# Optimization experiments

Hardware: AMD Instinct MI355X
Metric: run time of the kernel (lower is better)

## Reference

```python
import jax, jax.numpy as jnp
import numpy as np

C = 64          # channel multiplicity of node irreps (64x0e + 64x1o)
N = 10000       # nodes
E = 160000      # edges
F_EDGE = 8      # edge radial features (8x0e)
N_ELEM = 10     # one-hot element types (node_attrs, unused by this block)
WNUM = 4 * C    # conv_tp.weight_numel: 4 uvu instructions x 64 channels
SQ3 = float(np.sqrt(3.0))


def split_feats(x):
    # e3nn flat layout: [64 scalars | 64 vectors x 3 (u-major)]
    s = x[:, :C]
    v = x[:, C:].reshape(-1, C, 3)
    return s, v


def o3_linear(s, v, W0, W1):
    # per-irrep channel mixing with 1/sqrt(fan_in) normalization
    inv = 1.0 / float(np.sqrt(C))
    return (s @ W0) * inv, jnp.einsum('ncm,cd->ndm', v, W1) * inv


def fc_net(x, ws):
    # e3nn FullyConnectedNet: silu MLP with 1/sqrt(fan_in) scaling, no act on last
    for w in ws[:-1]:
        x = jax.nn.silu((x @ w) / float(np.sqrt(w.shape[0])))
    w = ws[-1]
    return (x @ w) / float(np.sqrt(w.shape[0]))


def setup_inputs() -> dict:
    key = jax.random.key(0)
    ks = jax.random.split(key, 16)
    inp = {}
    inp['node_attrs'] = jax.random.normal(ks[0], (N, N_ELEM), jnp.float32)
    inp['node_feats'] = jax.random.normal(ks[1], (N, C + 3 * C), jnp.float32)
    inp['edge_attrs'] = jax.random.normal(ks[2], (E, 4), jnp.float32)
    inp['edge_feats'] = jax.random.normal(ks[3], (E, F_EDGE), jnp.float32)
    inp['edge_index'] = jax.random.randint(ks[4], (2, E), 0, N, jnp.int32)
    inp['edge_vectors'] = jax.random.normal(ks[5], (E, 3), jnp.float32)
    inp['batch'] = jax.random.randint(ks[6], (N,), 0, 16, jnp.int32)
    inp['num_graphs'] = 16
    # learned params
    inp['W1_0'] = jax.random.normal(ks[7], (C, C), jnp.float32)
    inp['W1_1'] = jax.random.normal(ks[8], (C, C), jnp.float32)
    inp['W2_0'] = jax.random.normal(ks[9], (C, C), jnp.float32)
    inp['W2_1'] = jax.random.normal(ks[10], (C, C), jnp.float32)
    inp['fc_w0'] = jax.random.normal(ks[11], (F_EDGE, 64), jnp.float32)
    inp['fc_w1'] = jax.random.normal(ks[12], (64, 64), jnp.float32)
    inp['fc_w2'] = jax.random.normal(ks[13], (64, 64), jnp.float32)
    inp['fc_w3'] = jax.random.normal(ks[14], (64, WNUM), jnp.float32)
    k15, k16 = jax.random.split(ks[15])
    inp['Wf'] = jax.random.normal(k15, (2 * C, 1), jnp.float32)   # 128x0e mid -> 1x0e
    inp['Wm1'] = jax.random.normal(k16, (C, 1), jnp.float32)      # 64x1o -> 1x1o multipole
    return inp


def reference(node_attrs, node_feats, edge_attrs, edge_feats, edge_index,
              edge_vectors, batch, num_graphs,
              W1_0, W1_1, W2_0, W2_1, fc_w0, fc_w1, fc_w2, fc_w3, Wf, Wm1):
    sender = edge_index[0]
    receiver = edge_index[1]

    # per-edge tensor-product weights from radial features: [E, 4*C]
    tp_w = fc_net(edge_feats, [fc_w0, fc_w1, fc_w2, fc_w3])
    w0, w1, w2, w3 = (tp_w[:, 0 * C:1 * C], tp_w[:, 1 * C:2 * C],
                      tp_w[:, 2 * C:3 * C], tp_w[:, 3 * C:4 * C])

    s, v = split_feats(node_feats)
    s1, v1 = o3_linear(s, v, W1_0, W1_1)
    s2, v2 = o3_linear(s, v, W2_0, W2_1)

    # gather + symmetric bond features
    bs = s1[sender] + s2[receiver]          # [E, C] scalars
    bv = v1[sender] + v2[receiver]          # [E, C, 3] vectors

    y0 = edge_attrs[:, 0]                   # l=0 edge attr
    y1 = edge_attrs[:, 1:4]                 # l=1 edge attr

    # CG tensor product (uvu, shared_weights=False): only scalar (0e) outputs of
    # irreps_mid reach the final 1x0e o3.Linear, so the 1o paths drop out exactly.
    m0a = w0 * bs * y0[:, None]                                  # 0e x 0e -> 0e
    m0b = w3 * (jnp.einsum('ecm,em->ec', bv, y1) / SQ3)          # 1o x 1o -> 0e

    # final o3.Linear (128x0e -> 1x0e) and /40 scaling
    mid0 = jnp.concatenate([m0a, m0b], axis=-1)                  # [E, 2C]
    p_ji = (mid0 @ Wf)[:, 0] / float(np.sqrt(2 * C)) / 40.0      # [E]

    # double scatter-sum: antisymmetric charge transfer
    charges = (jax.ops.segment_sum(p_ji, receiver, num_segments=N)
               - jax.ops.segment_sum(p_ji, sender, num_segments=N))

    # multipole block: 0e component zeroed then overwritten by charges
    mvec = jnp.einsum('ncm,cd->ndm', v, Wm1)[:, 0, :] / float(np.sqrt(C))  # [N, 3]
    multipoles = jnp.concatenate([charges[:, None], mvec], axis=-1)        # [N, 4]

    return multipoles, p_ji[:, None]
```

## Files before the change

kernel.cpp:

```cpp
#include <hip/hip_runtime.h>
#include <hip/hip_bf16.h>

typedef float v4f __attribute__((ext_vector_type(4)));
typedef float f32x4 __attribute__((ext_vector_type(4)));
typedef unsigned short u16;
typedef unsigned short us4 __attribute__((ext_vector_type(4)));
typedef unsigned short us8 __attribute__((ext_vector_type(8)));
typedef short s16x8 __attribute__((ext_vector_type(8)));

#define N_NODES 10000
#define N_EDGES 160000

#define SWZ(idx, row) ((idx) ^ (((row) & 7) << 3))
#define GIDX(r, o) (((r) << 8) + (((((o) >> 3) ^ ((r) & 7))) << 3) + ((o) & 7))

__device__ __forceinline__ u16 f2b(float x) {
  union { float f; unsigned u; } v; v.f = x;
  unsigned r = v.u + 0x7fffu + ((v.u >> 16) & 1u);
  return (u16)(r >> 16);
}
__device__ __forceinline__ float b2f(u16 u) {
  union { unsigned u; float f; } v; v.u = ((unsigned)u) << 16; return v.f;
}
__device__ __forceinline__ float silu_f(float x) { return x / (1.0f + __expf(-x)); }

__device__ __forceinline__ void bar_lgkm() {
  asm volatile("s_waitcnt lgkmcnt(0)" ::: "memory");
  __builtin_amdgcn_s_barrier();
}

__device__ __forceinline__ void gload_lds16(const u16* g, u16* l) {
  __builtin_amdgcn_global_load_lds(
      (const __attribute__((address_space(1))) unsigned int*)g,
      (__attribute__((address_space(3))) unsigned int*)l, 16, 0, 0);
}

__global__ __launch_bounds__(256) void prep_kernel(
    const float* __restrict__ fcw0,
    const float* __restrict__ fcw1, const float* __restrict__ fcw2,
    const float* __restrict__ fcw3,
    const float* __restrict__ W10, const float* __restrict__ W20,
    const float* __restrict__ W11, const float* __restrict__ W21,
    u16* __restrict__ prep, float* __restrict__ out)
{
  const int fid = blockIdx.x * 256 + threadIdx.x;
  for (int i = fid; i < N_NODES; i += 4352) out[(size_t)i * 4] = 0.f;
  int f, sec;
  if (fid < 512)       { sec = 0; f = fid; }
  else if (fid < 1024) { sec = 1; f = fid - 512; }
  else if (fid < 2048) { sec = 2; f = fid - 1024; }
  else if (fid < 3072) { sec = 3; f = fid - 2048; }
  else if (fid < 4096) { sec = 4; f = fid - 3072; }
  else                 { sec = 5; f = fid - 4096; }
  const int lane = f & 63;
  us8 vals;
  if (sec == 5) {
    const int ut = f >> 6;
    #pragma unroll
    for (int j = 0; j < 8; ++j) {
      const int k = (lane >> 4) * 8 + j;
      vals[j] = (k < 8) ? f2b(fcw0[k * 64 + ut * 16 + (lane & 15)]) : (u16)0;
    }
  } else {
    const int kw = (f >> 6) & 1, ut = f >> 7;
    #pragma unroll
    for (int j = 0; j < 8; ++j) {
      const int k = kw * 32 + (lane >> 4) * 8 + j;
      float v;
      if (sec == 0) v = fcw1[k * 64 + ut * 16 + (lane & 15)];
      else if (sec == 1) v = fcw2[k * 64 + ut * 16 + (lane & 15)];
      else if (sec == 2) {
        const int col = (ut < 4) ? (ut * 16 + (lane & 15)) : (192 + (ut - 4) * 16 + (lane & 15));
        v = fcw3[k * 256 + col];
      } else if (sec == 3) {
        const int u = ut * 16 + (lane & 15);
        v = (u < 64) ? W10[k * 64 + u] : W20[k * 64 + (u - 64)];
      } else {
        const int u = ut * 16 + (lane & 15);
        v = (u < 64) ? W11[k * 64 + u] : W21[k * 64 + (u - 64)];
      }
      vals[j] = f2b(v);
    }
  }
  *(us8*)&prep[(size_t)fid * 8] = vals;
}

__global__ __launch_bounds__(256) void node_kernel(
    const float* __restrict__ nf,
    const u16* __restrict__ prepNS, const u16* __restrict__ prepNV,
    const float* __restrict__ Wm1,
    u16* __restrict__ Atab, u16* __restrict__ Btab, float* __restrict__ out)
{
  __shared__ u16 Ss[1024];
  __shared__ u16 Vs[3][1024];
  __shared__ float wm1s[64];
  const int tid = threadIdx.x, w = tid >> 6, lane = tid & 63;
  const int nb = blockIdx.x;

  if (tid < 64) wm1s[tid] = Wm1[tid];
  #pragma unroll
  for (int it = 0; it < 4; ++it) {
    const int flat = it * 1024 + tid * 4;
    const int nl = flat >> 8;
    const int col = flat & 255;
    const v4f x = *(const v4f*)&nf[((size_t)(nb * 16 + nl)) * 256 + col];
    #pragma unroll
    for (int i = 0; i < 4; ++i) {
      const int c2 = col + i;
      const u16 b = f2b(x[i]);
      if (c2 < 64) Ss[SWZ(nl * 64 + c2, nl)] = b;
      else {
        const int cc = c2 - 64, c = cc / 3, m = cc - c * 3;
        Vs[m][SWZ(nl * 64 + c, nl)] = b;
      }
    }
  }
  __syncthreads();

  const int nr = lane & 15, kg = (lane >> 4) * 8;
  const u16* plane = (w == 0) ? Ss : Vs[w - 1];
  const u16* pw = (w == 0) ? prepNS : prepNV;
  const s16x8 b0 = *(const s16x8*)&plane[SWZ(nr * 64 + kg, nr)];
  const s16x8 b1 = *(const s16x8*)&plane[SWZ(nr * 64 + 32 + kg, nr)];
  const int node = nb * 16 + nr;
  #pragma unroll
  for (int utg = 0; utg < 8; ++utg) {
    const s16x8 a0 = *(const s16x8*)&pw[((utg * 2 + 0) * 64 + lane) * 8];
    const s16x8 a1 = *(const s16x8*)&pw[((utg * 2 + 1) * 64 + lane) * 8];
    f32x4 acc = {0.f, 0.f, 0.f, 0.f};
    acc = __builtin_amdgcn_mfma_f32_16x16x32_bf16(a0, b0, acc, 0, 0, 0);
    acc = __builtin_amdgcn_mfma_f32_16x16x32_bf16(a1, b1, acc, 0, 0, 0);
    us4 st;
    #pragma unroll
    for (int j = 0; j < 4; ++j) st[j] = f2b(acc[j] * 0.125f);
    u16* tab = (utg < 4) ? Atab : Btab;
    const int ch = w * 64 + (utg & 3) * 16 + (lane >> 4) * 4;
    *(us4*)&tab[(size_t)node * 256 + ch] = st;
  }

  if (tid < 192) {
    const int task = tid >> 2, sub = tid & 3;
    const int nl3 = task / 3, m = task - nl3 * 3;
    float acc = 0.f;
    #pragma unroll
    for (int i = 0; i < 16; ++i) {
      const int c = sub * 16 + i;
      acc += b2f(Vs[m][SWZ(nl3 * 64 + c, nl3)]) * wm1s[c];
    }
    acc += __shfl_xor(acc, 1);
    acc += __shfl_xor(acc, 2);
    if (sub == 0) out[(nb * 16 + nl3) * 4 + 1 + m] = acc * 0.125f;
  }
}

__device__ __forceinline__ void mfma_layer32(const u16* Hin, u16* Hout,
                                             s16x8 a0, s16x8 a1, int w, int lane) {
  const int er = lane & 15, kg = (lane >> 4) * 8;
  __builtin_amdgcn_s_setprio(1);
  #pragma unroll
  for (int et = 0; et < 2; ++et) {
    const int e = et * 16 + er;
    const s16x8 b0 = *(const s16x8*)&Hin[SWZ(e * 64 + kg, e)];
    const s16x8 b1 = *(const s16x8*)&Hin[SWZ(e * 64 + 32 + kg, e)];
    f32x4 acc = {0.f, 0.f, 0.f, 0.f};
    acc = __builtin_amdgcn_mfma_f32_16x16x32_bf16(a0, b0, acc, 0, 0, 0);
    acc = __builtin_amdgcn_mfma_f32_16x16x32_bf16(a1, b1, acc, 0, 0, 0);
    us4 st;
    #pragma unroll
    for (int j = 0; j < 4; ++j) st[j] = f2b(silu_f(acc[j] * 0.125f));
    *(us4*)&Hout[SWZ(e * 64 + w * 16 + (lane >> 4) * 4, e)] = st;
  }
  __builtin_amdgcn_s_setprio(0);
}

__global__ __launch_bounds__(256, 2) void edge_kernel(
    const float* __restrict__ edge_attrs,
    const float* __restrict__ edge_feats,
    const int*   __restrict__ edge_index,
    const u16*   __restrict__ prep,
    const float* __restrict__ Wf,
    const u16*   __restrict__ Atab, const u16* __restrict__ Btab,
    float* __restrict__ out, float* __restrict__ p_out)
{
  __shared__ u16 G[2][16384];
  __shared__ u16 HA[2048], HB[2048];
  __shared__ u16 F16[256];
  __shared__ float yL[4][32];
  __shared__ float Psum[128];

  const int tid = threadIdx.x, w = tid >> 6, lane = tid & 63;
  const int half = lane >> 5, l31 = lane & 31;
  const int er = lane & 15, kg = (lane >> 4) * 8;
  const int cb = w * 16 + (lane >> 4) * 4;
  const int eb0 = blockIdx.x * 128;

  const u16* pL2 = prep;
  const u16* pL3 = prep + 512 * 8;
  const u16* pL4 = prep + 1024 * 8;
  const s16x8 a2_0 = *(const s16x8*)&pL2[((w * 2 + 0) * 64 + lane) * 8];
  const s16x8 a2_1 = *(const s16x8*)&pL2[((w * 2 + 1) * 64 + lane) * 8];
  const s16x8 a3_0 = *(const s16x8*)&pL3[((w * 2 + 0) * 64 + lane) * 8];
  const s16x8 a3_1 = *(const s16x8*)&pL3[((w * 2 + 1) * 64 + lane) * 8];
  const s16x8 as0 = *(const s16x8*)&pL4[((w * 2 + 0) * 64 + lane) * 8];
  const s16x8 as1 = *(const s16x8*)&pL4[((w * 2 + 1) * 64 + lane) * 8];
  const s16x8 av0 = *(const s16x8*)&pL4[(((4 + w) * 2 + 0) * 64 + lane) * 8];
  const s16x8 av1 = *(const s16x8*)&pL4[(((4 + w) * 2 + 1) * 64 + lane) * 8];
  const s16x8 a1w = *(const s16x8*)&prep[(size_t)(4096 + w * 64 + lane) * 8];
  const v4f wfA = *(const v4f*)&Wf[cb];
  v4f wfB = *(const v4f*)&Wf[64 + cb];
  #pragma unroll
  for (int j = 0; j < 4; ++j) wfB[j] *= 0.5773502691896258f;

  const u16* tabW = (w < 2) ? Atab : Btab;
  const int  eoff = (w < 2) ? 0 : N_EDGES;

  int nidx[2][8];
  int sndR[2], rcvR[2];
  v4f eaR[2], f0R[2], f1R[2];

  {
    #pragma unroll
    for (int i = 0; i < 8; ++i)
      nidx[0][i] = edge_index[eoff + eb0 + (w & 1) * 16 + 2 * i + half];
    if (tid < 32) {
      sndR[0] = edge_index[eb0 + tid];
      rcvR[0] = edge_index[N_EDGES + eb0 + tid];
      eaR[0] = *(const v4f*)&edge_attrs[(size_t)(eb0 + tid) * 4];
      f0R[0] = *(const v4f*)&edge_feats[(size_t)(eb0 + tid) * 8];
      f1R[0] = *(const v4f*)&edge_feats[(size_t)(eb0 + tid) * 8 + 4];
    }
    asm volatile("s_waitcnt vmcnt(0)" ::: "memory");
    #pragma unroll
    for (int i = 0; i < 8; ++i) {
      const int grow = w * 16 + 2 * i + half;
      const u16* src = tabW + (size_t)nidx[0][i] * 256 + (size_t)((l31 ^ (grow & 7)) << 3);
      gload_lds16(src, &G[0][(w * 16 + 2 * i) * 256]);
    }
    __builtin_amdgcn_sched_barrier(0);
    if (tid < 32) {
      yL[0][tid] = eaR[0][0]; yL[1][tid] = eaR[0][1];
      yL[2][tid] = eaR[0][2]; yL[3][tid] = eaR[0][3];
      us8 o;
      #pragma unroll
      for (int k = 0; k < 4; ++k) { o[k] = f2b(f0R[0][k]); o[4 + k] = f2b(f1R[0][k]); }
      *(us8*)&F16[tid * 8] = o;
    }
    bar_lgkm();
  }

  #pragma unroll
  for (int t = 0; t < 4; ++t) {
    const int cur = t & 1, nxt = cur ^ 1;
    const int eb = eb0 + t * 32;

    if (t < 3) {
      const int ebn = eb + 32;
      #pragma unroll
      for (int i = 0; i < 8; ++i)
        nidx[nxt][i] = edge_index[eoff + ebn + (w & 1) * 16 + 2 * i + half];
      if (tid < 32) {
        sndR[nxt] = edge_index[ebn + tid];
        rcvR[nxt] = edge_index[N_EDGES + ebn + tid];
        eaR[nxt] = *(const v4f*)&edge_attrs[(size_t)(ebn + tid) * 4];
        f0R[nxt] = *(const v4f*)&edge_feats[(size_t)(ebn + tid) * 8];
        f1R[nxt] = *(const v4f*)&edge_feats[(size_t)(ebn + tid) * 8 + 4];
      }
      __builtin_amdgcn_sched_barrier(0);
    }

    {
      __builtin_amdgcn_s_setprio(1);
      #pragma unroll
      for (int et = 0; et < 2; ++et) {
        s16x8 bF = {0, 0, 0, 0, 0, 0, 0, 0};
        if (lane < 16) bF = *(const s16x8*)&F16[(et * 16 + lane) * 8];
        f32x4 acc = {0.f, 0.f, 0.f, 0.f};
        acc = __builtin_amdgcn_mfma_f32_16x16x32_bf16(a1w, bF, acc, 0, 0, 0);
        const int e = et * 16 + er;
        us4 st;
        #pragma unroll
        for (int j = 0; j < 4; ++j)
          st[j] = f2b(silu_f(acc[j] * 0.35355339059327373f));
        *(us4*)&HA[SWZ(e * 64 + w * 16 + (lane >> 4) * 4, e)] = st;
      }
      __builtin_amdgcn_s_setprio(0);
    }
    bar_lgkm();
    mfma_layer32(HA, HB, a2_0, a2_1, w, lane);
    bar_lgkm();
    mfma_layer32(HB, HA, a3_0, a3_1, w, lane);
    bar_lgkm();

    f32x4 accS[2], accV[2];
    __builtin_amdgcn_s_setprio(1);
    #pragma unroll
    for (int et = 0; et < 2; ++et) {
      const int e = et * 16 + er;
      const s16x8 b0 = *(const s16x8*)&HA[SWZ(e * 64 + kg, e)];
      const s16x8 b1 = *(const s16x8*)&HA[SWZ(e * 64 + 32 + kg, e)];
      f32x4 aS = {0.f,0.f,0.f,0.f}, aV = {0.f,0.f,0.f,0.f};
      aS = __builtin_amdgcn_mfma_f32_16x16x32_bf16(as0, b0, aS, 0, 0, 0);
      aS = __builtin_amdgcn_mfma_f32_16x16x32_bf16(as1, b1, aS, 0, 0, 0);
      aV = __builtin_amdgcn_mfma_f32_16x16x32_bf16(av0, b0, aV, 0, 0, 0);
      aV = __builtin_amdgcn_mfma_f32_16x16x32_bf16(av1, b1, aV, 0, 0, 0);
      accS[et] = aS; accV[et] = aV;
    }
    __builtin_amdgcn_s_setprio(0);

    asm volatile("s_waitcnt vmcnt(0)" ::: "memory");
    if (t < 3) {
      #pragma unroll
      for (int i = 0; i < 8; ++i) {
        const int grow = w * 16 + 2 * i + half;
        const u16* src = tabW + (size_t)nidx[nxt][i] * 256 + (size_t)((l31 ^ (grow & 7)) << 3);
        gload_lds16(src, &G[nxt][(w * 16 + 2 * i) * 256]);
      }
      __builtin_amdgcn_sched_barrier(0);
    }
    __builtin_amdgcn_s_barrier();

    #pragma unroll
    for (int et = 0; et < 2; ++et) {
      const int e = et * 16 + er;
      const int rA = e, rB = 32 + e;
      const us4 As = *(const us4*)&G[cur][GIDX(rA, cb)];
      const us4 Ax = *(const us4*)&G[cur][GIDX(rA, 64 + cb)];
      const us4 Ay = *(const us4*)&G[cur][GIDX(rA, 128 + cb)];
      const us4 Az = *(const us4*)&G[cur][GIDX(rA, 192 + cb)];
      const us4 Bs = *(const us4*)&G[cur][GIDX(rB, cb)];
      const us4 Bx = *(const us4*)&G[cur][GIDX(rB, 64 + cb)];
      const us4 By = *(const us4*)&G[cur][GIDX(rB, 128 + cb)];
      const us4 Bz = *(const us4*)&G[cur][GIDX(rB, 192 + cb)];
      const float y0 = yL[0][e], yx = yL[1][e], yy = yL[2][e], yz = yL[3][e];
      float part = 0.f;
      #pragma unroll
      for (int j = 0; j < 4; ++j) {
        const float bs = b2f(As[j]) + b2f(Bs[j]);
        const float bv = (b2f(Ax[j]) + b2f(Bx[j])) * yx +
                         (b2f(Ay[j]) + b2f(By[j])) * yy +
                         (b2f(Az[j]) + b2f(Bz[j])) * yz;
        part += accS[et][j] * bs * y0 * wfA[j] + accV[et][j] * bv * wfB[j];
      }
      part += __shfl_xor(part, 16);
      part += __shfl_xor(part, 32);
      if (lane < 16) Psum[w * 32 + et * 16 + lane] = part;
    }
    bar_lgkm();
    if (tid < 32) {
      const float p = (Psum[tid] + Psum[32 + tid] + Psum[64 + tid] + Psum[96 + tid])
                      * 2.7621358640766505e-4f;
      p_out[eb + tid] = p;
      atomicAdd(&out[(size_t)rcvR[cur] * 4], p);
      atomicAdd(&out[(size_t)sndR[cur] * 4], -p);
      if (t < 3) {
        yL[0][tid] = eaR[nxt][0]; yL[1][tid] = eaR[nxt][1];
        yL[2][tid] = eaR[nxt][2]; yL[3][tid] = eaR[nxt][3];
        us8 o;
        #pragma unroll
        for (int k = 0; k < 4; ++k) { o[k] = f2b(f0R[nxt][k]); o[4 + k] = f2b(f1R[nxt][k]); }
        *(us8*)&F16[tid * 8] = o;
      }
    }
    bar_lgkm();
  }
}

extern "C" void kernel_launch(void* const* d_in, const int* in_sizes, int n_in,
                              void* d_out, int out_size, void* d_ws, size_t ws_size,
                              hipStream_t stream) {
  const float* node_feats = (const float*)d_in[1];
  const float* edge_attrs = (const float*)d_in[2];
  const float* edge_feats = (const float*)d_in[3];
  const int*   edge_index = (const int*)d_in[4];
  const float* W10  = (const float*)d_in[8];
  const float* W11  = (const float*)d_in[9];
  const float* W20  = (const float*)d_in[10];
  const float* W21  = (const float*)d_in[11];
  const float* fcw0 = (const float*)d_in[12];
  const float* fcw1 = (const float*)d_in[13];
  const float* fcw2 = (const float*)d_in[14];
  const float* fcw3 = (const float*)d_in[15];
  const float* Wf   = (const float*)d_in[16];
  const float* Wm1  = (const float*)d_in[17];
  float* out = (float*)d_out;

  char* ws = (char*)d_ws;
  u16* Atab = (u16*)ws;
  u16* Btab = (u16*)(ws + 5120000);
  u16* prep = (u16*)(ws + 10240000);

  prep_kernel<<<17, 256, 0, stream>>>(fcw0, fcw1, fcw2, fcw3, W10, W20, W11, W21,
                                      prep, out);
  node_kernel<<<625, 256, 0, stream>>>(node_feats, prep + 2048 * 8, prep + 3072 * 8,
                                       Wm1, Atab, Btab, out);
  edge_kernel<<<1250, 256, 0, stream>>>(edge_attrs, edge_feats, edge_index,
                                        prep, Wf, Atab, Btab,
                                        out, out + 40000);
}
```

Baseline: 156.3 us.

## Gather node rows directly into registers instead of double-buffered LDS staging

Removes the 64KB double-buffered LDS gather of per-edge sender/receiver table rows, which used global_load_lds. Each lane now loads only the 4-element slices it needs straight into registers at the start of each tile, and these loads overlap with the radial MLP MFMAs. This cuts LDS usage and one barrier per tile, which may allow higher occupancy. In exchange, prefetch is no longer one tile ahead: gather latency is hidden only within the same tile, and the scattered 8-byte loads are less coalesced than before.

```diff
diff --git a/kernel.cpp b/kernel.cpp
--- a/kernel.cpp
+++ b/kernel.cpp
@@ -12,7 +12,6 @@
 #define N_EDGES 160000
 
 #define SWZ(idx, row) ((idx) ^ (((row) & 7) << 3))
-#define GIDX(r, o) (((r) << 8) + (((((o) >> 3) ^ ((r) & 7))) << 3) + ((o) & 7))
 
 __device__ __forceinline__ u16 f2b(float x) {
   union { float f; unsigned u; } v; v.f = x;
@@ -27,12 +26,6 @@
 __device__ __forceinline__ void bar_lgkm() {
   asm volatile("s_waitcnt lgkmcnt(0)" ::: "memory");
   __builtin_amdgcn_s_barrier();
-}
-
-__device__ __forceinline__ void gload_lds16(const u16* g, u16* l) {
-  __builtin_amdgcn_global_load_lds(
-      (const __attribute__((address_space(1))) unsigned int*)g,
-      (__attribute__((address_space(3))) unsigned int*)l, 16, 0, 0);
 }
 
 __global__ __launch_bounds__(256) void prep_kernel(
@@ -182,14 +175,12 @@
     const u16*   __restrict__ Atab, const u16* __restrict__ Btab,
     float* __restrict__ out, float* __restrict__ p_out)
 {
-  __shared__ u16 G[2][16384];
   __shared__ u16 HA[2048], HB[2048];
   __shared__ u16 F16[256];
   __shared__ float yL[4][32];
   __shared__ float Psum[128];
 
   const int tid = threadIdx.x, w = tid >> 6, lane = tid & 63;
-  const int half = lane >> 5, l31 = lane & 31;
   const int er = lane & 15, kg = (lane >> 4) * 8;
   const int cb = w * 16 + (lane >> 4) * 4;
   const int eb0 = blockIdx.x * 128;
@@ -211,38 +202,28 @@
   #pragma unroll
   for (int j = 0; j < 4; ++j) wfB[j] *= 0.5773502691896258f;
 
-  const u16* tabW = (w < 2) ? Atab : Btab;
-  const int  eoff = (w < 2) ? 0 : N_EDGES;
-
-  int nidx[2][8];
+  int sndv[2][2], rcvv[2][2];
   int sndR[2], rcvR[2];
-  v4f eaR[2], f0R[2], f1R[2];
+  v4f eaR, f0R, f1R;
+  us4 gA[2][4], gB[2][4];
 
   {
     #pragma unroll
-    for (int i = 0; i < 8; ++i)
-      nidx[0][i] = edge_index[eoff + eb0 + (w & 1) * 16 + 2 * i + half];
+    for (int et = 0; et < 2; ++et) {
+      sndv[0][et] = edge_index[eb0 + et * 16 + er];
+      rcvv[0][et] = edge_index[N_EDGES + eb0 + et * 16 + er];
+    }
     if (tid < 32) {
       sndR[0] = edge_index[eb0 + tid];
       rcvR[0] = edge_index[N_EDGES + eb0 + tid];
-      eaR[0] = *(const v4f*)&edge_attrs[(size_t)(eb0 + tid) * 4];
-      f0R[0] = *(const v4f*)&edge_feats[(size_t)(eb0 + tid) * 8];
-      f1R[0] = *(const v4f*)&edge_feats[(size_t)(eb0 + tid) * 8 + 4];
-    }
-    asm volatile("s_waitcnt vmcnt(0)" ::: "memory");
-    #pragma unroll
-    for (int i = 0; i < 8; ++i) {
-      const int grow = w * 16 + 2 * i + half;
-      const u16* src = tabW + (size_t)nidx[0][i] * 256 + (size_t)((l31 ^ (grow & 7)) << 3);
-      gload_lds16(src, &G[0][(w * 16 + 2 * i) * 256]);
-    }
-    __builtin_amdgcn_sched_barrier(0);
-    if (tid < 32) {
-      yL[0][tid] = eaR[0][0]; yL[1][tid] = eaR[0][1];
-      yL[2][tid] = eaR[0][2]; yL[3][tid] = eaR[0][3];
+      eaR = *(const v4f*)&edge_attrs[(size_t)(eb0 + tid) * 4];
+      f0R = *(const v4f*)&edge_feats[(size_t)(eb0 + tid) * 8];
+      f1R = *(const v4f*)&edge_feats[(size_t)(eb0 + tid) * 8 + 4];
+      yL[0][tid] = eaR[0]; yL[1][tid] = eaR[1];
+      yL[2][tid] = eaR[2]; yL[3][tid] = eaR[3];
       us8 o;
       #pragma unroll
-      for (int k = 0; k < 4; ++k) { o[k] = f2b(f0R[0][k]); o[4 + k] = f2b(f1R[0][k]); }
+      for (int k = 0; k < 4; ++k) { o[k] = f2b(f0R[k]); o[4 + k] = f2b(f1R[k]); }
       *(us8*)&F16[tid * 8] = o;
     }
     bar_lgkm();
@@ -253,17 +234,31 @@
     const int cur = t & 1, nxt = cur ^ 1;
     const int eb = eb0 + t * 32;
 
+    #pragma unroll
+    for (int et = 0; et < 2; ++et) {
+      const u16* ra = Atab + (size_t)sndv[cur][et] * 256 + cb;
+      const u16* rb = Btab + (size_t)rcvv[cur][et] * 256 + cb;
+      #pragma unroll
+      for (int sec = 0; sec < 4; ++sec) {
+        gA[et][sec] = *(const us4*)&ra[sec * 64];
+        gB[et][sec] = *(const us4*)&rb[sec * 64];
+      }
+    }
+    __builtin_amdgcn_sched_barrier(0);
+
     if (t < 3) {
       const int ebn = eb + 32;
       #pragma unroll
-      for (int i = 0; i < 8; ++i)
-        nidx[nxt][i] = edge_index[eoff + ebn + (w & 1) * 16 + 2 * i + half];
+      for (int et = 0; et < 2; ++et) {
+        sndv[nxt][et] = edge_index[ebn + et * 16 + er];
+        rcvv[nxt][et] = edge_index[N_EDGES + ebn + et * 16 + er];
+      }
       if (tid < 32) {
         sndR[nxt] = edge_index[ebn + tid];
         rcvR[nxt] = edge_index[N_EDGES + ebn + tid];
-        eaR[nxt] = *(const v4f*)&edge_attrs[(size_t)(ebn + tid) * 4];
-        f0R[nxt] = *(const v4f*)&edge_feats[(size_t)(ebn + tid) * 8];
-        f1R[nxt] = *(const v4f*)&edge_feats[(size_t)(ebn + tid) * 8 + 4];
+        eaR = *(const v4f*)&edge_attrs[(size_t)(ebn + tid) * 4];
+        f0R = *(const v4f*)&edge_feats[(size_t)(ebn + tid) * 8];
+        f1R = *(const v4f*)&edge_feats[(size_t)(ebn + tid) * 8 + 4];
       }
       __builtin_amdgcn_sched_barrier(0);
     }
@@ -308,37 +303,18 @@
     __builtin_amdgcn_s_setprio(0);
 
     asm volatile("s_waitcnt vmcnt(0)" ::: "memory");
-    if (t < 3) {
-      #pragma unroll
-      for (int i = 0; i < 8; ++i) {
-        const int grow = w * 16 + 2 * i + half;
-        const u16* src = tabW + (size_t)nidx[nxt][i] * 256 + (size_t)((l31 ^ (grow & 7)) << 3);
-        gload_lds16(src, &G[nxt][(w * 16 + 2 * i) * 256]);
-      }
-      __builtin_amdgcn_sched_barrier(0);
-    }
-    __builtin_amdgcn_s_barrier();
 
     #pragma unroll
     for (int et = 0; et < 2; ++et) {
       const int e = et * 16 + er;
-      const int rA = e, rB = 32 + e;
-      const us4 As = *(const us4*)&G[cur][GIDX(rA, cb)];
-      const us4 Ax = *(const us4*)&G[cur][GIDX(rA, 64 + cb)];
-      const us4 Ay = *(const us4*)&G[cur][GIDX(rA, 128 + cb)];
-      const us4 Az = *(const us4*)&G[cur][GIDX(rA, 192 + cb)];
-      const us4 Bs = *(const us4*)&G[cur][GIDX(rB, cb)];
-      const us4 Bx = *(const us4*)&G[cur][GIDX(rB, 64 + cb)];
-      const us4 By = *(const us4*)&G[cur][GIDX(rB, 128 + cb)];
-      const us4 Bz = *(const us4*)&G[cur][GIDX(rB, 192 + cb)];
       const float y0 = yL[0][e], yx = yL[1][e], yy = yL[2][e], yz = yL[3][e];
       float part = 0.f;
       #pragma unroll
       for (int j = 0; j < 4; ++j) {
-        const float bs = b2f(As[j]) + b2f(Bs[j]);
-        const float bv = (b2f(Ax[j]) + b2f(Bx[j])) * yx +
-                         (b2f(Ay[j]) + b2f(By[j])) * yy +
-                         (b2f(Az[j]) + b2f(Bz[j])) * yz;
+        const float bs = b2f(gA[et][0][j]) + b2f(gB[et][0][j]);
+        const float bv = (b2f(gA[et][1][j]) + b2f(gB[et][1][j])) * yx +
+                         (b2f(gA[et][2][j]) + b2f(gB[et][2][j])) * yy +
+                         (b2f(gA[et][3][j]) + b2f(gB[et][3][j])) * yz;
         part += accS[et][j] * bs * y0 * wfA[j] + accV[et][j] * bv * wfB[j];
       }
       part += __shfl_xor(part, 16);
@@ -346,6 +322,7 @@
       if (lane < 16) Psum[w * 32 + et * 16 + lane] = part;
     }
     bar_lgkm();
+
     if (tid < 32) {
       const float p = (Psum[tid] + Psum[32 + tid] + Psum[64 + tid] + Psum[96 + tid])
                       * 2.7621358640766505e-4f;
@@ -353,11 +330,11 @@
       atomicAdd(&out[(size_t)rcvR[cur] * 4], p);
       atomicAdd(&out[(size_t)sndR[cur] * 4], -p);
       if (t < 3) {
-        yL[0][tid] = eaR[nxt][0]; yL[1][tid] = eaR[nxt][1];
-        yL[2][tid] = eaR[nxt][2]; yL[3][tid] = eaR[nxt][3];
+        yL[0][tid] = eaR[0]; yL[1][tid] = eaR[1];
+        yL[2][tid] = eaR[2]; yL[3][tid] = eaR[3];
         us8 o;
         #pragma unroll
-        for (int k = 0; k < 4; ++k) { o[k] = f2b(f0R[nxt][k]); o[4 + k] = f2b(f1R[nxt][k]); }
+        for (int k = 0; k < 4; ++k) { o[k] = f2b(f0R[k]); o[4 + k] = f2b(f1R[k]); }
         *(us8*)&F16[tid * 8] = o;
       }
     }
```

Result: slower. 166.2 us (+6.3%).

## Single-buffer gathered node tables in edge kernel and double tiles per block

Applied to the files above, without the earlier changes.

The gathered-node LDS buffer goes from two buffers to one, so each block uses about 32 KB less shared memory. The gather for the next tile is now issued only after the current tile's reads have finished. Each block also handles 8 edge tiles instead of 4, halving the grid to 625 blocks. The aim is higher occupancy from the smaller LDS footprint and less per-block setup, at the cost of losing overlap of the gather with the MFMA work inside one block, which now has to come from other resident blocks.

```diff
diff --git a/kernel.cpp b/kernel.cpp
--- a/kernel.cpp
+++ b/kernel.cpp
@@ -10,6 +10,7 @@
 
 #define N_NODES 10000
 #define N_EDGES 160000
+#define NTILE 8
 
 #define SWZ(idx, row) ((idx) ^ (((row) & 7) << 3))
 #define GIDX(r, o) (((r) << 8) + (((((o) >> 3) ^ ((r) & 7))) << 3) + ((o) & 7))
@@ -182,7 +183,7 @@
     const u16*   __restrict__ Atab, const u16* __restrict__ Btab,
     float* __restrict__ out, float* __restrict__ p_out)
 {
-  __shared__ u16 G[2][16384];
+  __shared__ u16 G[16384];
   __shared__ u16 HA[2048], HB[2048];
   __shared__ u16 F16[256];
   __shared__ float yL[4][32];
@@ -192,7 +193,7 @@
   const int half = lane >> 5, l31 = lane & 31;
   const int er = lane & 15, kg = (lane >> 4) * 8;
   const int cb = w * 16 + (lane >> 4) * 4;
-  const int eb0 = blockIdx.x * 128;
+  const int eb0 = blockIdx.x * (NTILE * 32);
 
   const u16* pL2 = prep;
   const u16* pL3 = prep + 512 * 8;
@@ -216,7 +217,7 @@
 
   int nidx[2][8];
   int sndR[2], rcvR[2];
-  v4f eaR[2], f0R[2], f1R[2];
+  v4f eaR, f0R, f1R;
 
   {
     #pragma unroll
@@ -225,35 +226,35 @@
     if (tid < 32) {
       sndR[0] = edge_index[eb0 + tid];
       rcvR[0] = edge_index[N_EDGES + eb0 + tid];
-      eaR[0] = *(const v4f*)&edge_attrs[(size_t)(eb0 + tid) * 4];
-      f0R[0] = *(const v4f*)&edge_feats[(size_t)(eb0 + tid) * 8];
-      f1R[0] = *(const v4f*)&edge_feats[(size_t)(eb0 + tid) * 8 + 4];
+      eaR = *(const v4f*)&edge_attrs[(size_t)(eb0 + tid) * 4];
+      f0R = *(const v4f*)&edge_feats[(size_t)(eb0 + tid) * 8];
+      f1R = *(const v4f*)&edge_feats[(size_t)(eb0 + tid) * 8 + 4];
     }
     asm volatile("s_waitcnt vmcnt(0)" ::: "memory");
     #pragma unroll
     for (int i = 0; i < 8; ++i) {
       const int grow = w * 16 + 2 * i + half;
       const u16* src = tabW + (size_t)nidx[0][i] * 256 + (size_t)((l31 ^ (grow & 7)) << 3);
-      gload_lds16(src, &G[0][(w * 16 + 2 * i) * 256]);
+      gload_lds16(src, &G[(w * 16 + 2 * i) * 256]);
     }
     __builtin_amdgcn_sched_barrier(0);
     if (tid < 32) {
-      yL[0][tid] = eaR[0][0]; yL[1][tid] = eaR[0][1];
-      yL[2][tid] = eaR[0][2]; yL[3][tid] = eaR[0][3];
+      yL[0][tid] = eaR[0]; yL[1][tid] = eaR[1];
+      yL[2][tid] = eaR[2]; yL[3][tid] = eaR[3];
       us8 o;
       #pragma unroll
-      for (int k = 0; k < 4; ++k) { o[k] = f2b(f0R[0][k]); o[4 + k] = f2b(f1R[0][k]); }
+      for (int k = 0; k < 4; ++k) { o[k] = f2b(f0R[k]); o[4 + k] = f2b(f1R[k]); }
       *(us8*)&F16[tid * 8] = o;
     }
     bar_lgkm();
   }
 
   #pragma unroll
-  for (int t = 0; t < 4; ++t) {
+  for (int t = 0; t < NTILE; ++t) {
     const int cur = t & 1, nxt = cur ^ 1;
     const int eb = eb0 + t * 32;
 
-    if (t < 3) {
+    if (t < NTILE - 1) {
       const int ebn = eb + 32;
       #pragma unroll
       for (int i = 0; i < 8; ++i)
@@ -261,9 +262,9 @@
       if (tid < 32) {
         sndR[nxt] = edge_index[ebn + tid];
         rcvR[nxt] = edge_index[N_EDGES + ebn + tid];
-        eaR[nxt] = *(const v4f*)&edge_attrs[(size_t)(ebn + tid) * 4];
-        f0R[nxt] = *(const v4f*)&edge_feats[(size_t)(ebn + tid) * 8];
-        f1R[nxt] = *(const v4f*)&edge_feats[(size_t)(ebn + tid) * 8 + 4];
+        eaR = *(const v4f*)&edge_attrs[(size_t)(ebn + tid) * 4];
+        f0R = *(const v4f*)&edge_feats[(size_t)(ebn + tid) * 8];
+        f1R = *(const v4f*)&edge_feats[(size_t)(ebn + tid) * 8 + 4];
       }
       __builtin_amdgcn_sched_barrier(0);
     }
@@ -308,29 +309,20 @@
     __builtin_amdgcn_s_setprio(0);
 
     asm volatile("s_waitcnt vmcnt(0)" ::: "memory");
-    if (t < 3) {
-      #pragma unroll
-      for (int i = 0; i < 8; ++i) {
-        const int grow = w * 16 + 2 * i + half;
-        const u16* src = tabW + (size_t)nidx[nxt][i] * 256 + (size_t)((l31 ^ (grow & 7)) << 3);
-        gload_lds16(src, &G[nxt][(w * 16 + 2 * i) * 256]);
-      }
-      __builtin_amdgcn_sched_barrier(0);
-    }
     __builtin_amdgcn_s_barrier();
 
     #pragma unroll
     for (int et = 0; et < 2; ++et) {
       const int e = et * 16 + er;
       const int rA = e, rB = 32 + e;
-      const us4 As = *(const us4*)&G[cur][GIDX(rA, cb)];
-      const us4 Ax = *(const us4*)&G[cur][GIDX(rA, 64 + cb)];
-      const us4 Ay = *(const us4*)&G[cur][GIDX(rA, 128 + cb)];
-      const us4 Az = *(const us4*)&G[cur][GIDX(rA, 192 + cb)];
-      const us4 Bs = *(const us4*)&G[cur][GIDX(rB, cb)];
-      const us4 Bx = *(const us4*)&G[cur][GIDX(rB, 64 + cb)];
-      const us4 By = *(const us4*)&G[cur][GIDX(rB, 128 + cb)];
-      const us4 Bz = *(const us4*)&G[cur][GIDX(rB, 192 + cb)];
+      const us4 As = *(const us4*)&G[GIDX(rA, cb)];
+      const us4 Ax = *(const us4*)&G[GIDX(rA, 64 + cb)];
+      const us4 Ay = *(const us4*)&G[GIDX(rA, 128 + cb)];
+      const us4 Az = *(const us4*)&G[GIDX(rA, 192 + cb)];
+      const us4 Bs = *(const us4*)&G[GIDX(rB, cb)];
+      const us4 Bx = *(const us4*)&G[GIDX(rB, 64 + cb)];
+      const us4 By = *(const us4*)&G[GIDX(rB, 128 + cb)];
+      const us4 Bz = *(const us4*)&G[GIDX(rB, 192 + cb)];
       const float y0 = yL[0][e], yx = yL[1][e], yy = yL[2][e], yz = yL[3][e];
       float part = 0.f;
       #pragma unroll
@@ -346,18 +338,29 @@
       if (lane < 16) Psum[w * 32 + et * 16 + lane] = part;
     }
     bar_lgkm();
+
+    if (t < NTILE - 1) {
+      #pragma unroll
+      for (int i = 0; i < 8; ++i) {
+        const int grow = w * 16 + 2 * i + half;
+        const u16* src = tabW + (size_t)nidx[nxt][i] * 256 + (size_t)((l31 ^ (grow & 7)) << 3);
+        gload_lds16(src, &G[(w * 16 + 2 * i) * 256]);
+      }
+      __builtin_amdgcn_sched_barrier(0);
+    }
+
     if (tid < 32) {
       const float p = (Psum[tid] + Psum[32 + tid] + Psum[64 + tid] + Psum[96 + tid])
                       * 2.7621358640766505e-4f;
       p_out[eb + tid] = p;
       atomicAdd(&out[(size_t)rcvR[cur] * 4], p);
       atomicAdd(&out[(size_t)sndR[cur] * 4], -p);
-      if (t < 3) {
-        yL[0][tid] = eaR[nxt][0]; yL[1][tid] = eaR[nxt][1];
-        yL[2][tid] = eaR[nxt][2]; yL[3][tid] = eaR[nxt][3];
+      if (t < NTILE - 1) {
+        yL[0][tid] = eaR[0]; yL[1][tid] = eaR[1];
+        yL[2][tid] = eaR[2]; yL[3][tid] = eaR[3];
         us8 o;
         #pragma unroll
-        for (int k = 0; k < 4; ++k) { o[k] = f2b(f0R[nxt][k]); o[4 + k] = f2b(f1R[nxt][k]); }
+        for (int k = 0; k < 4; ++k) { o[k] = f2b(f0R[k]); o[4 + k] = f2b(f1R[k]); }
         *(us8*)&F16[tid * 8] = o;
       }
     }
@@ -393,7 +396,7 @@
                                       prep, out);
   node_kernel<<<625, 256, 0, stream>>>(node_feats, prep + 2048 * 8, prep + 3072 * 8,
                                        Wm1, Atab, Btab, out);
-  edge_kernel<<<1250, 256, 0, stream>>>(edge_attrs, edge_feats, edge_index,
-                                        prep, Wf, Atab, Btab,
-                                        out, out + 40000);
-}
+  edge_kernel<<<625, 256, 0, stream>>>(edge_attrs, edge_feats, edge_index,
+                                       prep, Wf, Atab, Btab,
+                                       out, out + 40000);
+}
```

Result: faster. 145.5 us (-6.9%).
